# Kernel optimization log

Hardware: AMD Instinct MI355X
Metric: run time of the kernel (lower is better)

The kernel has to match this reference:

```python
import jax, jax.numpy as jnp
import numpy as np

B, S, T, E, H, VIN, VOUT = 64, 64, 32, 512, 1024, 32000, 32000


def setup_inputs() -> dict:
    key = jax.random.key(0)
    ks = jax.random.split(key, 12)
    rn = lambda k, shape, s=0.02: jax.random.normal(k, shape, jnp.float32) * s
    return {
        "src": jax.random.randint(ks[0], (B, S), 0, VIN),
        "tgt": jax.random.randint(ks[1], (B, T), 0, VOUT),
        "enc_emb": rn(ks[2], (VIN, E)),
        "dec_emb": rn(ks[3], (VOUT, E)),
        "enc_Wih": rn(ks[4], (4 * H, E)),
        "enc_Whh": rn(ks[5], (4 * H, H)),
        "enc_bih": jnp.zeros((4 * H,), jnp.float32),
        "enc_bhh": jnp.zeros((4 * H,), jnp.float32),
        "dec_Wih": rn(ks[6], (4 * H, E + H)),
        "dec_Whh": rn(ks[7], (4 * H, H)),
        "dec_bih": jnp.zeros((4 * H,), jnp.float32),
        "dec_bhh": jnp.zeros((4 * H,), jnp.float32),
        "attn_W": rn(ks[8], (H, 2 * H)),
        "attn_b": jnp.zeros((H,), jnp.float32),
        "v": jax.random.uniform(ks[9], (H,), jnp.float32),
        "fc_W": rn(ks[10], (VOUT, 2 * H)),
        "fc_b": jnp.zeros((VOUT,), jnp.float32),
    }


def _lstm_cell(x, h, c, Wih, Whh, bih, bhh):
    # torch gate order: i, f, g, o
    gates = x @ Wih.T + bih + h @ Whh.T + bhh
    i, f, g, o = jnp.split(gates, 4, axis=-1)
    c_new = jax.nn.sigmoid(f) * c + jax.nn.sigmoid(i) * jnp.tanh(g)
    h_new = jax.nn.sigmoid(o) * jnp.tanh(c_new)
    return h_new, c_new


def _forward(src, tgt, enc_emb, dec_emb, enc_Wih, enc_Whh, enc_bih, enc_bhh,
             dec_Wih, dec_Whh, dec_bih, dec_bhh, attn_W, attn_b, v, fc_W, fc_b):
    b, s = src.shape
    t_len = tgt.shape[1]
    hdim = enc_Whh.shape[1]

    # ---- encoder (single-layer LSTM, batch_first) ----
    x = enc_emb[src]  # [B,S,E] (dropout=0 in eval)

    def enc_step(carry, x_t):
        h, c = carry
        h, c = _lstm_cell(x_t, h, c, enc_Wih, enc_Whh, enc_bih, enc_bhh)
        return (h, c), h

    h0 = jnp.zeros((b, hdim), x.dtype)
    (h_f, c_f), enc_out_tm = jax.lax.scan(enc_step, (h0, h0), jnp.swapaxes(x, 0, 1))
    enc_out = jnp.swapaxes(enc_out_tm, 0, 1)  # [B,S,H]

    # hidden.detach() in torch
    h_f = jax.lax.stop_gradient(h_f)
    c_f = jax.lax.stop_gradient(c_f)

    # split attn_W for the concat(hidden, enc_out) linear
    Wh, We = attn_W[:, :hdim], attn_W[:, hdim:]
    enc_proj = jnp.einsum('bsh,kh->bsk', enc_out, We)  # hoisted, [B,S,H]

    def dec_step(carry, tok):
        h, c = carry
        emb = dec_emb[tok]  # [B,E]
        # Bahdanau attention: tanh(Linear(cat(h, enc_out))) . v
        energy = jnp.tanh(h @ Wh.T[None] if False else jnp.tanh((h @ Wh.T)[:, None, :] + enc_proj + attn_b))
        energy = jnp.tanh((h @ Wh.T)[:, None, :] + enc_proj + attn_b)  # [B,S,H]
        scores = jnp.einsum('bsh,h->bs', energy, v)
        a = jax.nn.softmax(scores, axis=1)
        context = jnp.einsum('bs,bsh->bh', a, enc_out)  # [B,H]
        rnn_in = jnp.concatenate([emb, context], axis=-1)
        h_new, c_new = _lstm_cell(rnn_in, h, c, dec_Wih, dec_Whh, dec_bih, dec_bhh)
        logits = jnp.concatenate([h_new, context], axis=-1) @ fc_W.T + fc_b
        return (h_new, c_new), logits

    # teacher_forcing_ratio = 1.0 -> input at step t is tgt[:, t-1]
    toks_tm = jnp.swapaxes(tgt[:, : t_len - 1], 0, 1)  # [T-1, B]
    _, logits_tm = jax.lax.scan(dec_step, (h_f, c_f), toks_tm)  # [T-1,B,V]
    logits = jnp.swapaxes(logits_tm, 0, 1)  # [B,T-1,V]
    zeros0 = jnp.zeros((b, 1, fc_W.shape[0]), logits.dtype)
    return jnp.concatenate([zeros0, logits], axis=1)  # [B,T,V]


def reference(src, tgt, enc_emb, dec_emb, enc_Wih, enc_Whh, enc_bih, enc_bhh,
              dec_Wih, dec_Whh, dec_bih, dec_bhh, attn_W, attn_b, v, fc_W, fc_b):
    return _forward(src, tgt, enc_emb, dec_emb, enc_Wih, enc_Whh, enc_bih, enc_bhh,
                    dec_Wih, dec_Whh, dec_bih, dec_bhh, attn_W, attn_b, v, fc_W, fc_b)
```

## Files before the change

kernel.cpp:

```cpp
#include <hip/hip_runtime.h>
#include <hip/hip_bf16.h>

typedef __bf16 bf16x8 __attribute__((ext_vector_type(8)));
typedef float  f32x4  __attribute__((ext_vector_type(4)));
typedef _Float16 h16x8 __attribute__((ext_vector_type(8)));

__device__ __forceinline__ unsigned short f2b(float f) {
    union { float f; unsigned u; } w; w.f = f;
    unsigned u = w.u + 0x7FFF + ((w.u >> 16) & 1);
    return (unsigned short)(u >> 16);
}
__device__ __forceinline__ float tanhfast(float x) {
    float e = __expf(2.0f * x);
    return 1.0f - 2.0f / (e + 1.0f);
}

__device__ __forceinline__ void stU(unsigned* p, unsigned v) {
    __hip_atomic_store(p, v, __ATOMIC_RELAXED, __HIP_MEMORY_SCOPE_SYSTEM);
}
__device__ __forceinline__ void stF(float* p, float v) {
    __hip_atomic_store(p, v, __ATOMIC_RELAXED, __HIP_MEMORY_SCOPE_SYSTEM);
}
__device__ __forceinline__ int ldI(const int* p) {
    return __hip_atomic_load((int*)p, __ATOMIC_RELAXED, __HIP_MEMORY_SCOPE_SYSTEM);
}
__device__ __forceinline__ void stI(int* p, int v) {
    __hip_atomic_store(p, v, __ATOMIC_RELAXED, __HIP_MEMORY_SCOPE_SYSTEM);
}

#define GLD16(g, l) __builtin_amdgcn_global_load_lds( \
    (const __attribute__((address_space(1))) void*)(g), \
    (__attribute__((address_space(3))) void*)(l), 16, 0, 0)

#define SLOT_STRIDE 16

__device__ __forceinline__ void gbar(int* slots, int* gen, int target) {
    asm volatile("s_waitcnt vmcnt(0)" ::: "memory");
    __syncthreads();
    if (blockIdx.x == 0) {
        if (threadIdx.x == 0) stI(slots, target);
        while (ldI(slots + threadIdx.x * SLOT_STRIDE) < target)
            __builtin_amdgcn_s_sleep(1);
        __syncthreads();
        if (threadIdx.x == 0) stI(gen, target);
    } else {
        if (threadIdx.x == 0) {
            stI(slots + blockIdx.x * SLOT_STRIDE, target);
            while (ldI(gen) < target)
                __builtin_amdgcn_s_sleep(1);
        }
        __syncthreads();
    }
}

__device__ __forceinline__ void mac8(const unsigned short* A, const unsigned short* B,
                                     f32x4& acc) {
    bf16x8 a[8], b[8];
#pragma unroll
    for (int kk = 0; kk < 8; ++kk) {
        a[kk] = *(const bf16x8*)(A + kk * 32);
        b[kk] = *(const bf16x8*)(B + kk * 32);
    }
#pragma unroll
    for (int kk = 0; kk < 8; ++kk)
        acc = __builtin_amdgcn_mfma_f32_16x16x32_bf16(a[kk], b[kk], acc, 0, 0, 0);
}


__global__ void k_gather(const float* __restrict__ emb, const int* __restrict__ tok,
                         unsigned short* __restrict__ out, int L, int ldtok) {
    long total = (long)L * 64 * 128;
    for (long i = (long)blockIdx.x * blockDim.x + threadIdx.x; i < total;
         i += (long)gridDim.x * blockDim.x) {
        int  e4 = (int)(i & 127);
        long r  = i >> 7;
        int  t  = (int)(r >> 6), b = (int)(r & 63);
        int  tk = tok[b * ldtok + t];
        float4 v = *(const float4*)(emb + (long)tk * 512 + e4 * 4);
        ushort4 o; o.x = f2b(v.x); o.y = f2b(v.y); o.z = f2b(v.z); o.w = f2b(v.w);
        *(ushort4*)(out + r * 512 + e4 * 4) = o;
    }
}

__global__ void k_conv(const float* __restrict__ in, unsigned short* __restrict__ out,
                       long N_, int K_, int ldin, int col0, int ldout, int outcol0, int reorder) {
    long total = N_ * (K_ >> 2);
    int kq = K_ >> 2;
    for (long i = (long)blockIdx.x * blockDim.x + threadIdx.x; i < total;
         i += (long)gridDim.x * blockDim.x) {
        long n = i / kq;
        int  k4 = (int)(i - n * kq) * 4;
        long row = reorder ? (long)((n & 3) * 1024 + (n >> 2)) : n;
        float4 v = *(const float4*)(in + row * ldin + col0 + k4);
        ushort4 o; o.x = f2b(v.x); o.y = f2b(v.y); o.z = f2b(v.z); o.w = f2b(v.w);
        *(ushort4*)(out + n * ldout + outcol0 + k4) = o;
    }
}

__global__ void k_bias(const float* __restrict__ b1, const float* __restrict__ b2,
                       float* __restrict__ out) {
    int n = blockIdx.x * blockDim.x + threadIdx.x;
    if (n < 4096) {
        int row = (n & 3) * 1024 + (n >> 2);
        out[n] = b1[row] + b2[row];
    }
}

__global__ void k_zero0(float* __restrict__ out) {
    long total = 64L * 8000;
    for (long i = (long)blockIdx.x * blockDim.x + threadIdx.x; i < total;
         i += (long)gridDim.x * blockDim.x) {
        int b = (int)(i / 8000), q = (int)(i % 8000);
        float4 z = {0.f, 0.f, 0.f, 0.f};
        *(float4*)(out + (long)b * 1024000 + q * 4) = z;
    }
}

template<int BM, int BN, int WGM, int WGN, int FM, int FN>
__device__ __forceinline__ void gemm_core(
    const unsigned short* __restrict__ A, int lda,
    const unsigned short* __restrict__ B, int ldb,
    long m0, long n0, int K,
    unsigned short* As, unsigned short* Bs,
    f32x4 (&acc)[FM][FN])
{
    const int tid  = threadIdx.x;
    const int lane = tid & 63;
    const int wave = tid >> 6;
    const int wm = wave / WGN;
    const int wn = wave % WGN;
    const int srow = lane >> 2;
    const int scol = (lane & 3) * 8;
    const int frow = lane & 15;
    const int fcol = (lane >> 4) * 8;

    for (int k0 = 0; k0 < K; k0 += 32) {
        __syncthreads();
        for (int c = wave; c < BM / 16; c += 4) {
            const unsigned short* g = A + (m0 + c * 16 + srow) * (long)lda + k0 + scol;
            GLD16(g, As + c * 512);
        }
        for (int c = wave; c < BN / 16; c += 4) {
            const unsigned short* g = B + (n0 + c * 16 + srow) * (long)ldb + k0 + scol;
            GLD16(g, Bs + c * 512);
        }
        __syncthreads();
        bf16x8 af[FM], bfr[FN];
#pragma unroll
        for (int m = 0; m < FM; ++m)
            af[m] = *(const bf16x8*)(As + ((wm * FM + m) * 16 + frow) * 32 + fcol);
#pragma unroll
        for (int n = 0; n < FN; ++n)
            bfr[n] = *(const bf16x8*)(Bs + ((wn * FN + n) * 16 + frow) * 32 + fcol);
#pragma unroll
        for (int m = 0; m < FM; ++m)
#pragma unroll
            for (int n = 0; n < FN; ++n)
                acc[m][n] = __builtin_amdgcn_mfma_f32_16x16x32_bf16(af[m], bfr[n], acc[m][n], 0, 0, 0);
    }
}

template<int BM, int BN, int WGM, int WGN, int FM, int FN, int MODE>
__global__ __launch_bounds__(256) void k_gemm(
    const unsigned short* __restrict__ A, int lda,
    const unsigned short* __restrict__ B, int ldb,
    float* __restrict__ C, long ldc, const float* __restrict__ bias,
    int M, int N, int K, int Mreal)
{
    __shared__ __align__(16) unsigned short As[BM * 32];
    __shared__ __align__(16) unsigned short Bs[BN * 32];
    long m0 = (long)blockIdx.y * BM;
    long n0 = (long)blockIdx.x * BN;
    f32x4 acc[FM][FN] = {};
    gemm_core<BM, BN, WGM, WGN, FM, FN>(A, lda, B, ldb, m0, n0, K, As, Bs, acc);

    const int lane = threadIdx.x & 63;
    const int wave = threadIdx.x >> 6;
    const int wm = wave / WGN, wn = wave % WGN;
#pragma unroll
    for (int n = 0; n < FN; ++n) {
        long col = n0 + wn * FN * 16 + n * 16 + (lane & 15);
        float bv = bias ? bias[col] : 0.0f;
#pragma unroll
        for (int m = 0; m < FM; ++m) {
            int rl = wm * FM * 16 + m * 16 + (lane >> 4) * 4;
#pragma unroll
            for (int q = 0; q < 4; ++q) {
                long r = m0 + rl + q;
                float val = acc[m][n][q] + bv;
                if (MODE == 0) {
                    C[r * ldc + col] = val;
                } else if (MODE == 2) {
                    ((_Float16*)C)[r * ldc + col] = (_Float16)val;
                } else {
                    if (r < Mreal) {
                        long orow = (r & 63) * 32 + (r >> 6) + 1;
                        C[orow * ldc + col] = val;
                    }
                }
            }
        }
    }
}

__global__ __launch_bounds__(256) void k_enc(
    const unsigned short* __restrict__ W,
    const float* __restrict__ pre,
    unsigned short* __restrict__ hsl,
    unsigned short* __restrict__ enc_out,
    unsigned short* __restrict__ eoT,
    unsigned short* __restrict__ hS0,
    float* __restrict__ cspill,
    int* slots, int* gen)
{
    __shared__ float gs[64 * 16];
    const int blk = blockIdx.x, tid = threadIdx.x;
    const int lane = tid & 63, wave = tid >> 6;
    const int n0 = blk * 16;
    const int arow = wave * 16 + (lane & 15);
    const int kch = (lane >> 4) * 8;
    const unsigned short* Bw = W + (long)(n0 + (lane & 15)) * 1024 + kch;
    const int pb = tid >> 1, pjl = (tid & 1) * 2;
    const int jg = blk * 4 + pjl;
    float c0 = 0.f, c1 = 0.f;
    float4 pr0 = {}, pr1 = {};
    if (tid < 128) {
        pr0 = *(const float4*)(pre + (long)pb * 4096 + n0 + pjl * 4);
        pr1 = *(const float4*)(pre + (long)pb * 4096 + n0 + pjl * 4 + 4);
    }
    int bt = 0;
    for (int t = 0; t < 64; ++t) {
        const unsigned short* Ar = hsl + (long)t * 65536 + (long)arow * 1024 + kch;
        f32x4 acc = {};
        mac8(Ar, Bw, acc);
        mac8(Ar + 256, Bw + 256, acc);
        mac8(Ar + 512, Bw + 512, acc);
        mac8(Ar + 768, Bw + 768, acc);
#pragma unroll
        for (int q = 0; q < 4; ++q)
            gs[(wave * 16 + (lane >> 4) * 4 + q) * 16 + (lane & 15)] = acc[q];
        __syncthreads();
        if (tid < 128) {
            float4 gA = *(const float4*)(gs + pb * 16 + pjl * 4);
            float4 gB = *(const float4*)(gs + pb * 16 + pjl * 4 + 4);
            float h0v, h1v;
            {
                float gi = gA.x + pr0.x, gf = gA.y + pr0.y, gg = gA.z + pr0.z, go = gA.w + pr0.w;
                float i_ = 1.f / (1.f + __expf(-gi)), f_ = 1.f / (1.f + __expf(-gf));
                float g_ = tanhfast(gg), o_ = 1.f / (1.f + __expf(-go));
                c0 = f_ * c0 + i_ * g_; h0v = o_ * tanhfast(c0);
            }
            {
                float gi = gB.x + pr1.x, gf = gB.y + pr1.y, gg = gB.z + pr1.z, go = gB.w + pr1.w;
                float i_ = 1.f / (1.f + __expf(-gi)), f_ = 1.f / (1.f + __expf(-gf));
                float g_ = tanhfast(gg), o_ = 1.f / (1.f + __expf(-go));
                c1 = f_ * c1 + i_ * g_; h1v = o_ * tanhfast(c1);
            }
            unsigned short hb0 = f2b(h0v), hb1 = f2b(h1v);
            unsigned pk = (unsigned)hb0 | ((unsigned)hb1 << 16);
            stU((unsigned*)(hsl + (long)(t + 1) * 65536 + (long)pb * 1024 + jg), pk);
            *(unsigned*)(enc_out + ((long)pb * 64 + t) * 1024 + jg) = pk;
            eoT[((long)pb * 1024 + jg) * 64 + t]     = hb0;
            eoT[((long)pb * 1024 + jg + 1) * 64 + t] = hb1;
            if (t < 63) {
                pr0 = *(const float4*)(pre + (long)(t + 1) * 262144 + (long)pb * 4096 + n0 + pjl * 4);
                pr1 = *(const float4*)(pre + (long)(t + 1) * 262144 + (long)pb * 4096 + n0 + pjl * 4 + 4);
            } else {
                *(unsigned*)(hS0 + (long)pb * 1024 + jg) = pk;
                cspill[(long)pb * 1024 + jg]     = c0;
                cspill[(long)pb * 1024 + jg + 1] = c1;
            }
        }
        gbar(slots, gen, ++bt);
    }
}

__global__ __launch_bounds__(256) void k_dec(
    const unsigned short* __restrict__ Wh,
    const unsigned short* __restrict__ Wc,
    const float* __restrict__ pre,
    const _Float16* __restrict__ proj16,
    const unsigned short* __restrict__ eoT,
    const float* __restrict__ v,
    const float* __restrict__ cspill,
    unsigned short* __restrict__ hS,
    unsigned short* __restrict__ ctxS,
    float* __restrict__ qS,
    unsigned short* __restrict__ fcin,
    int* slots, int* gen)
{
    __shared__ float gs[64 * 16];
    __shared__ float qv[1024], vv[1024];
    __shared__ float sc[64], al[64];
    const int blk = blockIdx.x, tid = threadIdx.x;
    const int lane = tid & 63, wave = tid >> 6;
    const int n0 = blk * 16;
    const int arow = wave * 16 + (lane & 15);
    const int kch = (lane >> 4) * 8;
    const int pb = tid >> 1, pjl = (tid & 1) * 2;
    const int jg = blk * 4 + pjl;
    {
        float4 v4 = *(const float4*)(v + tid * 4);
        *(float4*)(vv + tid * 4) = v4;
    }
    float c0 = 0.f, c1 = 0.f;
    if (tid < 128) {
        c0 = cspill[(long)pb * 1024 + jg];
        c1 = cspill[(long)pb * 1024 + jg + 1];
    }
    __syncthreads();
    int bt = 0;
    for (int t = 0; t < 31; ++t) {
        const unsigned short* hSt   = hS   + (long)t * 65536;
        const unsigned short* ctxSt = ctxS + (long)t * 65536;
        float4 pr0 = {}, pr1 = {};
        if (tid < 128) {
            pr0 = *(const float4*)(pre + (long)t * 262144 + (long)pb * 4096 + n0 + pjl * 4);
            pr1 = *(const float4*)(pre + (long)t * 262144 + (long)pb * 4096 + n0 + pjl * 4 + 4);
        }
        if (blk < 64) {
            const unsigned short* Ar = hSt + (long)arow * 1024 + kch;
            const unsigned short* Bq = Wh + (long)(blk * 16 + (lane & 15)) * 1024 + kch;
            f32x4 qa = {};
            mac8(Ar, Bq, qa);
            mac8(Ar + 256, Bq + 256, qa);
            mac8(Ar + 512, Bq + 512, qa);
            mac8(Ar + 768, Bq + 768, qa);
#pragma unroll
            for (int q = 0; q < 4; ++q)
                gs[(wave * 16 + (lane >> 4) * 4 + q) * 16 + (lane & 15)] = qa[q];
            __syncthreads();
            int b = tid >> 2, cl = (tid & 3) * 4;
            float* qd = qS + (long)t * 65536 + (long)b * 1024 + blk * 16 + cl;
#pragma unroll
            for (int g = 0; g < 4; ++g) stF(qd + g, gs[b * 16 + cl + g]);
        }
        gbar(slots, gen, ++bt);
        if (blk < 64) {
            const int b = blk;
            *(float4*)(qv + tid * 4) = *(const float4*)(qS + (long)t * 65536 + (long)b * 1024 + tid * 4);
            __syncthreads();
            int s = tid >> 2, part = tid & 3;
            const h16x8* pp = (const h16x8*)(proj16 + ((long)b * 64 + s) * 1024 + part * 256);
            float a_ = 0.f;
#pragma unroll 4
            for (int d = 0; d < 32; ++d) {
                h16x8 pv = pp[d];
                int h = part * 256 + d * 8;
#pragma unroll
                for (int j = 0; j < 8; ++j)
                    a_ += vv[h + j] * tanhfast(qv[h + j] + (float)pv[j]);
            }
            a_ += __shfl_xor(a_, 1);
            a_ += __shfl_xor(a_, 2);
            if (part == 0) sc[s] = a_;
            __syncthreads();
            if (tid < 64) {
                float x = sc[tid], mx = x;
                for (int o = 32; o; o >>= 1) mx = fmaxf(mx, __shfl_xor(mx, o));
                float e = __expf(x - mx), su = e;
                for (int o = 32; o; o >>= 1) su += __shfl_xor(su, o);
                al[tid] = e / su;
            }
            __syncthreads();
            int h0 = tid * 4;
            float cacc[4];
#pragma unroll
            for (int r = 0; r < 4; ++r) {
                const bf16x8* ep = (const bf16x8*)(eoT + ((long)b * 1024 + h0 + r) * 64);
                float s_ = 0.f;
#pragma unroll
                for (int c8 = 0; c8 < 8; ++c8) {
                    bf16x8 v8 = ep[c8];
#pragma unroll
                    for (int jj = 0; jj < 8; ++jj)
                        s_ += al[c8 * 8 + jj] * (float)v8[jj];
                }
                cacc[r] = s_;
            }
            unsigned pk0 = (unsigned)f2b(cacc[0]) | ((unsigned)f2b(cacc[1]) << 16);
            unsigned pk1 = (unsigned)f2b(cacc[2]) | ((unsigned)f2b(cacc[3]) << 16);
            stU((unsigned*)(ctxS + (long)t * 65536 + (long)b * 1024 + h0), pk0);
            stU((unsigned*)(ctxS + (long)t * 65536 + (long)b * 1024 + h0 + 2), pk1);
            *(unsigned*)(fcin + ((long)t * 64 + b) * 2048 + 1024 + h0)     = pk0;
            *(unsigned*)(fcin + ((long)t * 64 + b) * 2048 + 1024 + h0 + 2) = pk1;
        }
        gbar(slots, gen, ++bt);
        {
            const unsigned short* Ah = hSt   + (long)arow * 1024 + kch;
            const unsigned short* Ac = ctxSt + (long)arow * 1024 + kch;
            const unsigned short* Bw = Wc + (long)(n0 + (lane & 15)) * 2048 + kch;
            f32x4 acc = {};
            mac8(Ah,       Bw,        acc);
            mac8(Ah + 256, Bw + 256,  acc);
            mac8(Ah + 512, Bw + 512,  acc);
            mac8(Ah + 768, Bw + 768,  acc);
            mac8(Ac,       Bw + 1024, acc);
            mac8(Ac + 256, Bw + 1280, acc);
            mac8(Ac + 512, Bw + 1536, acc);
            mac8(Ac + 768, Bw + 1792, acc);
#pragma unroll
            for (int q = 0; q < 4; ++q)
                gs[(wave * 16 + (lane >> 4) * 4 + q) * 16 + (lane & 15)] = acc[q];
            __syncthreads();
            if (tid < 128) {
                float4 gA = *(const float4*)(gs + pb * 16 + pjl * 4);
                float4 gB = *(const float4*)(gs + pb * 16 + pjl * 4 + 4);
                float h0v, h1v;
                {
                    float gi = gA.x + pr0.x, gf = gA.y + pr0.y, gg = gA.z + pr0.z, go = gA.w + pr0.w;
                    float i_ = 1.f / (1.f + __expf(-gi)), f_ = 1.f / (1.f + __expf(-gf));
                    float g_ = tanhfast(gg), o_ = 1.f / (1.f + __expf(-go));
                    c0 = f_ * c0 + i_ * g_; h0v = o_ * tanhfast(c0);
                }
                {
                    float gi = gB.x + pr1.x, gf = gB.y + pr1.y, gg = gB.z + pr1.z, go = gB.w + pr1.w;
                    float i_ = 1.f / (1.f + __expf(-gi)), f_ = 1.f / (1.f + __expf(-gf));
                    float g_ = tanhfast(gg), o_ = 1.f / (1.f + __expf(-go));
                    c1 = f_ * c1 + i_ * g_; h1v = o_ * tanhfast(c1);
                }
                unsigned pk = (unsigned)f2b(h0v) | ((unsigned)f2b(h1v) << 16);
                stU((unsigned*)(hS + (long)(t + 1) * 65536 + (long)pb * 1024 + jg), pk);
                *(unsigned*)(fcin + ((long)t * 64 + pb) * 2048 + jg) = pk;
            }
        }
        gbar(slots, gen, ++bt);
    }
}

extern "C" void kernel_launch(void* const* d_in, const int* in_sizes, int n_in,
                              void* d_out, int out_size, void* d_ws, size_t ws_size,
                              hipStream_t stream) {
    const int*   src     = (const int*)d_in[0];
    const int*   tgt     = (const int*)d_in[1];
    const float* enc_emb = (const float*)d_in[2];
    const float* dec_emb = (const float*)d_in[3];
    const float* enc_Wih = (const float*)d_in[4];
    const float* enc_Whh = (const float*)d_in[5];
    const float* enc_bih = (const float*)d_in[6];
    const float* enc_bhh = (const float*)d_in[7];
    const float* dec_Wih = (const float*)d_in[8];
    const float* dec_Whh = (const float*)d_in[9];
    const float* dec_bih = (const float*)d_in[10];
    const float* dec_bhh = (const float*)d_in[11];
    const float* attn_W  = (const float*)d_in[12];
    const float* attn_b  = (const float*)d_in[13];
    const float* vvec    = (const float*)d_in[14];
    const float* fc_W    = (const float*)d_in[15];
    const float* fc_b    = (const float*)d_in[16];
    float* out = (float*)d_out;

    char* ws = (char*)d_ws;
    size_t off = 0;
    auto alloc = [&](size_t bytes) -> char* {
        off = (off + 255) & ~(size_t)255;
        char* p = ws + off; off += bytes; return p;
    };
    unsigned short* wX      = (unsigned short*)alloc(4096UL * 512 * 2);
    unsigned short* weWih   = (unsigned short*)alloc(4096UL * 512 * 2);
    unsigned short* weWhh   = (unsigned short*)alloc(4096UL * 1024 * 2);
    float*          ebias   = (float*)alloc(4096UL * 4);
    float*          pre_enc = (float*)alloc(4096UL * 4096 * 4);
    unsigned short* enc_out = (unsigned short*)alloc(4096UL * 1024 * 2);
    unsigned short* eoT     = (unsigned short*)alloc(64UL * 1024 * 64 * 2);
    unsigned short* wWe     = (unsigned short*)alloc(1024UL * 1024 * 2);
    unsigned short* wWh     = (unsigned short*)alloc(1024UL * 1024 * 2);
    _Float16*       proj16  = (_Float16*)alloc(4096UL * 1024 * 2);
    float*          cbuf    = (float*)alloc(64UL * 1024 * 4);
    unsigned short* demb    = (unsigned short*)alloc(2048UL * 512 * 2);
    unsigned short* wDemb   = (unsigned short*)alloc(4096UL * 512 * 2);
    unsigned short* wCat    = (unsigned short*)alloc(4096UL * 2048 * 2);
    float*          dbias   = (float*)alloc(4096UL * 4);
    float*          pre_dec = (float*)alloc(2048UL * 4096 * 4);
    unsigned short* fcin    = (unsigned short*)alloc(2048UL * 2048 * 2);
    unsigned short* wFc     = (unsigned short*)alloc(32000UL * 2048 * 2);
    unsigned short* hslE    = (unsigned short*)alloc(65UL * 65536 * 2);
    unsigned short* hS      = (unsigned short*)alloc(32UL * 65536 * 2);
    unsigned short* ctxS    = (unsigned short*)alloc(32UL * 65536 * 2);
    float*          qS      = (float*)alloc(32UL * 65536 * 4);
    int*            bar     = (int*)alloc(65536);
    (void)ws_size; (void)in_sizes; (void)n_in; (void)out_size;

    int* slotsE = bar;
    int* genE   = bar + 4096;
    int* slotsD = bar + 8192;
    int* genD   = bar + 12288;

    hipMemsetAsync(bar, 0, 65536, stream);
    hipMemsetAsync(hslE, 0, 65536UL * 2, stream);
    k_zero0<<<512, 256, 0, stream>>>(out);

    k_gather<<<2048, 256, 0, stream>>>(enc_emb, src, wX, 64, 64);
    k_gather<<<1024, 256, 0, stream>>>(dec_emb, tgt, demb, 31, 32);
    k_conv<<<2048, 256, 0, stream>>>(enc_Wih, weWih, 4096, 512, 512, 0, 512, 0, 1);
    k_conv<<<2048, 256, 0, stream>>>(enc_Whh, weWhh, 4096, 1024, 1024, 0, 1024, 0, 1);
    k_conv<<<2048, 256, 0, stream>>>(dec_Wih, wDemb, 4096, 512, 1536, 0, 512, 0, 1);
    k_conv<<<2048, 256, 0, stream>>>(dec_Whh, wCat, 4096, 1024, 1024, 0, 2048, 0, 1);
    k_conv<<<2048, 256, 0, stream>>>(dec_Wih, wCat, 4096, 1024, 1536, 512, 2048, 1024, 1);
    k_conv<<<2048, 256, 0, stream>>>(attn_W, wWh, 1024, 1024, 2048, 0, 1024, 0, 0);
    k_conv<<<2048, 256, 0, stream>>>(attn_W, wWe, 1024, 1024, 2048, 1024, 1024, 0, 0);
    k_conv<<<4096, 256, 0, stream>>>(fc_W, wFc, 32000, 2048, 2048, 0, 2048, 0, 0);
    k_bias<<<16, 256, 0, stream>>>(enc_bih, enc_bhh, ebias);
    k_bias<<<16, 256, 0, stream>>>(dec_bih, dec_bhh, dbias);

    k_gemm<128,128,2,2,4,4,0><<<dim3(32, 32), 256, 0, stream>>>(
        wX, 512, weWih, 512, pre_enc, 4096, ebias, 4096, 4096, 512, 4096);
    k_gemm<128,128,2,2,4,4,0><<<dim3(32, 16), 256, 0, stream>>>(
        demb, 512, wDemb, 512, pre_dec, 4096, dbias, 2048, 4096, 512, 2048);

    k_enc<<<256, 256, 0, stream>>>(weWhh, pre_enc, hslE, enc_out, eoT,
                                   hS, cbuf, slotsE, genE);

    k_gemm<128,128,2,2,4,4,2><<<dim3(8, 32), 256, 0, stream>>>(
        enc_out, 1024, wWe, 1024, (float*)proj16, 1024, attn_b, 4096, 1024, 1024, 4096);

    k_dec<<<256, 256, 0, stream>>>(wWh, wCat, pre_dec, proj16, eoT, vvec, cbuf,
                                   hS, ctxS, qS, fcin, slotsD, genD);

    k_gemm<128,128,2,2,4,4,1><<<dim3(250, 16), 256, 0, stream>>>(
        fcin, 2048, wFc, 2048, out, 32000, fc_b, 2048, 32000, 2048, 1984);
}
```

Before: 2.822 ms.

## Narrow atomic scope, swizzle FC GEMM blocks, spread decoder query GEMV over all blocks

```diff
diff --git a/kernel.cpp b/kernel.cpp
--- a/kernel.cpp
+++ b/kernel.cpp
@@ -16,16 +16,16 @@
 }
 
 __device__ __forceinline__ void stU(unsigned* p, unsigned v) {
-    __hip_atomic_store(p, v, __ATOMIC_RELAXED, __HIP_MEMORY_SCOPE_SYSTEM);
+    __hip_atomic_store(p, v, __ATOMIC_RELAXED, __HIP_MEMORY_SCOPE_AGENT);
 }
 __device__ __forceinline__ void stF(float* p, float v) {
-    __hip_atomic_store(p, v, __ATOMIC_RELAXED, __HIP_MEMORY_SCOPE_SYSTEM);
+    __hip_atomic_store(p, v, __ATOMIC_RELAXED, __HIP_MEMORY_SCOPE_AGENT);
 }
 __device__ __forceinline__ int ldI(const int* p) {
-    return __hip_atomic_load((int*)p, __ATOMIC_RELAXED, __HIP_MEMORY_SCOPE_SYSTEM);
+    return __hip_atomic_load((int*)p, __ATOMIC_RELAXED, __HIP_MEMORY_SCOPE_AGENT);
 }
 __device__ __forceinline__ void stI(int* p, int v) {
-    __hip_atomic_store(p, v, __ATOMIC_RELAXED, __HIP_MEMORY_SCOPE_SYSTEM);
+    __hip_atomic_store(p, v, __ATOMIC_RELAXED, __HIP_MEMORY_SCOPE_AGENT);
 }
 
 #define GLD16(g, l) __builtin_amdgcn_global_load_lds( \
@@ -169,8 +169,16 @@
 {
     __shared__ __align__(16) unsigned short As[BM * 32];
     __shared__ __align__(16) unsigned short Bs[BN * 32];
-    long m0 = (long)blockIdx.y * BM;
-    long n0 = (long)blockIdx.x * BN;
+    long m0, n0;
+    if (MODE == 1) {
+        int bid = blockIdx.x;
+        int n = (bid & 7) * 32 + (bid >> 7);
+        int m = (bid >> 3) & 15;
+        if (n >= 250) return;
+        m0 = (long)m * BM; n0 = (long)n * BN;
+    } else {
+        m0 = (long)blockIdx.y * BM; n0 = (long)blockIdx.x * BN;
+    }
     f32x4 acc[FM][FN] = {};
     gemm_core<BM, BN, WGM, WGN, FM, FN>(A, lda, B, ldb, m0, n0, K, As, Bs, acc);
 
@@ -318,22 +326,20 @@
             pr0 = *(const float4*)(pre + (long)t * 262144 + (long)pb * 4096 + n0 + pjl * 4);
             pr1 = *(const float4*)(pre + (long)t * 262144 + (long)pb * 4096 + n0 + pjl * 4 + 4);
         }
-        if (blk < 64) {
-            const unsigned short* Ar = hSt + (long)arow * 1024 + kch;
-            const unsigned short* Bq = Wh + (long)(blk * 16 + (lane & 15)) * 1024 + kch;
+        {
+            int nq = blk >> 2, mt = blk & 3;
+            gs[tid] = 0.f;
+            __syncthreads();
+            const unsigned short* Ar = hSt + (long)(mt * 16 + (lane & 15)) * 1024 + wave * 256 + kch;
+            const unsigned short* Bq = Wh + (long)(nq * 16 + (lane & 15)) * 1024 + wave * 256 + kch;
             f32x4 qa = {};
             mac8(Ar, Bq, qa);
-            mac8(Ar + 256, Bq + 256, qa);
-            mac8(Ar + 512, Bq + 512, qa);
-            mac8(Ar + 768, Bq + 768, qa);
 #pragma unroll
             for (int q = 0; q < 4; ++q)
-                gs[(wave * 16 + (lane >> 4) * 4 + q) * 16 + (lane & 15)] = qa[q];
+                atomicAdd(&gs[((lane >> 4) * 4 + q) * 16 + (lane & 15)], qa[q]);
             __syncthreads();
-            int b = tid >> 2, cl = (tid & 3) * 4;
-            float* qd = qS + (long)t * 65536 + (long)b * 1024 + blk * 16 + cl;
-#pragma unroll
-            for (int g = 0; g < 4; ++g) stF(qd + g, gs[b * 16 + cl + g]);
+            stF(qS + (long)t * 65536 + (long)(mt * 16 + (tid >> 4)) * 1024 + nq * 16 + (tid & 15),
+                gs[tid]);
         }
         gbar(slots, gen, ++bt);
         if (blk < 64) {
@@ -517,6 +523,6 @@
     k_dec<<<256, 256, 0, stream>>>(wWh, wCat, pre_dec, proj16, eoT, vvec, cbuf,
                                    hS, ctxS, qS, fcin, slotsD, genD);
 
-    k_gemm<128,128,2,2,4,4,1><<<dim3(250, 16), 256, 0, stream>>>(
+    k_gemm<128,128,2,2,4,4,1><<<dim3(4096), 256, 0, stream>>>(
         fcin, 2048, wFc, 2048, out, 32000, fc_b, 2048, 32000, 2048, 1984);
 }
```

After: 2.680 ms. -5.0%, faster.
